# Kernel optimization log

Measured on AMD Instinct MI355X. Metric: run time of the kernel, lower is better.

## Reference

```python
import jax, jax.numpy as jnp
import numpy as np

BETA = 0.1
GAMMA = 0.5
LABEL_SMOOTHING = 0.0
IGNORE_INDEX = -100

B, T, H, V = 8, 512, 2048, 32000  # B = 2 * num_pairs (first half chosen, second half rejected)


def setup_inputs() -> dict:
    key = jax.random.key(0)
    k1, k2, k3, k4 = jax.random.split(key, 4)
    lin_weight = jax.random.normal(k1, (V, H), dtype=jnp.float32) * 0.02
    _input = jax.random.normal(k2, (B, T, H), dtype=jnp.float32)
    target = jax.random.randint(k3, (B, T), 0, V, dtype=jnp.int64)
    # sprinkle some ignore_index positions like padded labels
    pad = jax.random.uniform(k4, (B, T)) < 0.1
    target = jnp.where(pad, IGNORE_INDEX, target)
    bias = jax.random.normal(k4, (V,), dtype=jnp.float32) * 0.02
    return {"lin_weight": lin_weight, "_input": _input, "target": target, "bias": bias}


def reference(lin_weight, _input, target, bias):
    # fused linear -> log_softmax over vocab
    logits = jnp.einsum("bth,vh->btv", _input, lin_weight) + bias  # (B, T, V)
    logps = jax.nn.log_softmax(logits.astype(jnp.float32), axis=-1)
    # gather target log-probs, masking ignore_index
    mask = (target != IGNORE_INDEX)
    tgt = jnp.where(mask, target, 0)
    per_token_logps = jnp.take_along_axis(logps, tgt[..., None], axis=-1)[..., 0]
    per_token_logps = per_token_logps * mask  # (B, T)
    # SimPO uses length-normalized (average) sequence log-prob
    avg_logps = per_token_logps.sum(-1) / jnp.maximum(mask.sum(-1), 1)  # (B,)
    n_pairs = B // 2
    chosen_logps = avg_logps[:n_pairs]
    rejected_logps = avg_logps[n_pairs:]
    d = BETA * (chosen_logps - rejected_logps) - GAMMA
    loss = (-jax.nn.log_sigmoid(d) * (1.0 - LABEL_SMOOTHING)
            - jax.nn.log_sigmoid(-d) * LABEL_SMOOTHING).sum() / n_pairs
    return loss
```

## Files before the change

### kernel.cpp

```cpp
#include <hip/hip_runtime.h>
#include <stdint.h>
#include <math.h>

constexpr int Bb = 8, Tt = 512, Hh = 2048, Vv = 32000;
constexpr int M = Bb * Tt;
constexpr int K = Hh;
constexpr int N = Vv;
constexpr int BM = 256, BN = 256, BK = 64;
constexpr int MBLK = M / BM;
constexpr int NBLK = N / BN;
constexpr int KTILES = K / BK;
constexpr int IGNORE = -100;

typedef __attribute__((ext_vector_type(8))) short bf16x8;
typedef __attribute__((ext_vector_type(4))) float f32x4;
typedef __attribute__((ext_vector_type(4))) unsigned short u16x4;

__device__ inline void gld16(const void* g, void* l) {
  __builtin_amdgcn_global_load_lds(
      (const __attribute__((address_space(1))) uint32_t*)g,
      (__attribute__((address_space(3))) uint32_t*)l, 16, 0, 0);
}

__device__ __forceinline__ void barrier_f() {
  asm volatile("" ::: "memory");
  __builtin_amdgcn_s_barrier();
  asm volatile("" ::: "memory");
}

__device__ inline unsigned short f2bf(float f) {
  union { float f; unsigned u; } x; x.f = f;
  unsigned r = x.u + 0x7fffu + ((x.u >> 16) & 1u);
  return (unsigned short)(r >> 16);
}

constexpr int NX4 = M * K / 4;
constexpr int NW4 = N * K / 4;
__global__ __launch_bounds__(256)
void cast_fused(const float* __restrict__ Xf, unsigned short* __restrict__ Xb,
                const float* __restrict__ Wf, unsigned short* __restrict__ Wb) {
  int64_t i = (int64_t)blockIdx.x * blockDim.x + threadIdx.x;
  const int64_t stride = (int64_t)gridDim.x * blockDim.x;
  for (; i < (int64_t)NX4 + NW4; i += stride) {
    const f32x4* s4;
    u16x4* d4;
    int64_t j;
    if (i < NX4) { s4 = (const f32x4*)Xf; d4 = (u16x4*)Xb; j = i; }
    else         { s4 = (const f32x4*)Wf; d4 = (u16x4*)Wb; j = i - NX4; }
    f32x4 v = __builtin_nontemporal_load(&s4[j]);
    u16x4 o;
    o[0] = f2bf(v[0]); o[1] = f2bf(v[1]); o[2] = f2bf(v[2]); o[3] = f2bf(v[3]);
    d4[j] = o;
  }
}


template <int BUF, int KS, int MH, int VM, class STG>
__device__ __forceinline__ void phase(const unsigned short* __restrict__ AsB,
                                      const unsigned short* __restrict__ BsB,
                                      const int* offA, const int* offB,
                                      bf16x8 (&bfrag)[4], f32x4 (&acc)[8][4],
                                      STG&& stg) {
  const unsigned short* Ab = AsB + (BUF * 2 + KS) * 8192;
  if (MH == 0) {
    const unsigned short* Bp = BsB + (BUF * 2 + KS) * 8192;
#pragma unroll
    for (int nf = 0; nf < 4; ++nf) bfrag[nf] = *(const bf16x8*)(Bp + offB[nf]);
  }
  bf16x8 af[4];
#pragma unroll
  for (int mi = 0; mi < 4; ++mi) af[mi] = *(const bf16x8*)(Ab + offA[MH * 4 + mi]);
  stg();
  if (VM == 8) asm volatile("s_waitcnt vmcnt(8)" ::: "memory");
  if (VM == 4) asm volatile("s_waitcnt vmcnt(4)" ::: "memory");
  if (VM == 0) asm volatile("s_waitcnt vmcnt(0)" ::: "memory");
  barrier_f();
  asm volatile("s_waitcnt lgkmcnt(0)" ::: "memory");
  __builtin_amdgcn_s_setprio(1);
#pragma unroll
  for (int mi = 0; mi < 4; ++mi)
#pragma unroll
    for (int nf = 0; nf < 4; ++nf)
      acc[MH * 4 + mi][nf] = __builtin_amdgcn_mfma_f32_16x16x32_bf16(
          af[mi], bfrag[nf], acc[MH * 4 + mi][nf], 0, 0, 0);
  __builtin_amdgcn_s_setprio(0);
  barrier_f();
}

__global__ __launch_bounds__(512, 2)
void gemm_stats(const unsigned short* __restrict__ X,
                const unsigned short* __restrict__ W,
                const float* __restrict__ bias,
                const int* __restrict__ tgt,
                float* __restrict__ m_part,
                float* __restrict__ s_part,
                float* __restrict__ tlogit) {
  extern __shared__ unsigned short smem[];
  unsigned short* AsB = smem;
  unsigned short* BsB = smem + 32768;
  float* red_m = (float*)(smem + 65536);
  float* red_s = red_m + 1024;

  const int tid = threadIdx.x;
  const int lane = tid & 63;
  const int wid = tid >> 6;
  const int waveM = wid >> 2;
  const int waveN = wid & 3;
  const int q = lane >> 4;
  const int c = lane & 15;

  const int swz = (blockIdx.x & 7) * (MBLK * NBLK / 8) + (blockIdx.x >> 3);
  const int bm = swz & (MBLK - 1);
  const int bn = swz >> 4;

  const int srow = tid >> 2;
  const int sch = (lane & 3) ^ ((lane >> 3) & 3);
  const unsigned short* gA = X + (size_t)(bm * BM + srow) * K + sch * 8;
  const unsigned short* gB = W + (size_t)(bn * BN + srow) * K + sch * 8;
  unsigned short* const dA0 = AsB + wid * 512;
  unsigned short* const dB0 = BsB + wid * 512;

  auto stA = [&](int b, int h, int t) {
    const unsigned short* s = gA + t * BK + h * 32;
    unsigned short* d = dA0 + (b * 2 + h) * 8192;
    gld16(s, d);
    gld16(s + (size_t)128 * K, d + 4096);
  };
  auto stB = [&](int b, int h, int t) {
    const unsigned short* s = gB + t * BK + h * 32;
    unsigned short* d = dB0 + (b * 2 + h) * 8192;
    gld16(s, d);
    gld16(s + (size_t)128 * K, d + 4096);
  };

  const int chrd = (q ^ ((c >> 1) & 3)) * 8;
  int offA[8], offB[4];
#pragma unroll
  for (int mf = 0; mf < 8; ++mf) offA[mf] = (waveM * 128 + mf * 16 + c) * 32 + chrd;
#pragma unroll
  for (int nf = 0; nf < 4; ++nf) offB[nf] = (waveN * 64 + nf * 16 + c) * 32 + chrd;

  f32x4 acc[8][4];
#pragma unroll
  for (int i = 0; i < 8; ++i)
#pragma unroll
    for (int j = 0; j < 4; ++j) acc[i][j] = (f32x4){0.f, 0.f, 0.f, 0.f};
  bf16x8 bfrag[4];

  stA(0, 0, 0); stB(0, 0, 0);
  stA(0, 1, 0); stB(0, 1, 0);
  stA(1, 0, 1); stB(1, 0, 1);
  asm volatile("s_waitcnt vmcnt(8)" ::: "memory");
  barrier_f();

  for (int i = 0; i < KTILES / 2 - 1; ++i) {
    const int t0 = 2 * i;
    phase<0, 0, 0, -1>(AsB, BsB, offA, offB, bfrag, acc, [&] { stA(1, 1, t0 + 1); });
    phase<0, 0, 1,  8>(AsB, BsB, offA, offB, bfrag, acc, [&] { stB(1, 1, t0 + 1); });
    phase<0, 1, 0, -1>(AsB, BsB, offA, offB, bfrag, acc, [&] { stA(0, 0, t0 + 2); });
    phase<0, 1, 1,  8>(AsB, BsB, offA, offB, bfrag, acc, [&] { stB(0, 0, t0 + 2); });
    phase<1, 0, 0, -1>(AsB, BsB, offA, offB, bfrag, acc, [&] { stA(0, 1, t0 + 2); });
    phase<1, 0, 1,  8>(AsB, BsB, offA, offB, bfrag, acc, [&] { stB(0, 1, t0 + 2); });
    phase<1, 1, 0, -1>(AsB, BsB, offA, offB, bfrag, acc, [&] { stA(1, 0, t0 + 3); });
    phase<1, 1, 1,  8>(AsB, BsB, offA, offB, bfrag, acc, [&] { stB(1, 0, t0 + 3); });
  }
  {
    auto nop = [&] {};
    phase<0, 0, 0, -1>(AsB, BsB, offA, offB, bfrag, acc, [&] { stA(1, 1, KTILES - 1); });
    phase<0, 0, 1,  8>(AsB, BsB, offA, offB, bfrag, acc, [&] { stB(1, 1, KTILES - 1); });
    phase<0, 1, 0, -1>(AsB, BsB, offA, offB, bfrag, acc, nop);
    phase<0, 1, 1,  4>(AsB, BsB, offA, offB, bfrag, acc, nop);
    phase<1, 0, 0, -1>(AsB, BsB, offA, offB, bfrag, acc, nop);
    phase<1, 0, 1,  0>(AsB, BsB, offA, offB, bfrag, acc, nop);
    phase<1, 1, 0, -1>(AsB, BsB, offA, offB, bfrag, acc, nop);
    phase<1, 1, 1, -1>(AsB, BsB, offA, offB, bfrag, acc, nop);
  }

  const int colBase = bn * BN + waveN * 64;
  float bvals[4];
#pragma unroll
  for (int nf = 0; nf < 4; ++nf) bvals[nf] = bias[colBase + nf * 16 + c];

#pragma unroll
  for (int mf = 0; mf < 8; ++mf) {
    const int rowBase = bm * BM + waveM * 128 + mf * 16 + q * 4;
#pragma unroll
    for (int reg = 0; reg < 4; ++reg) {
      const int grow = rowBase + reg;
      const int t = tgt[grow];
      float v[4];
      float mloc = -3.4e38f;
#pragma unroll
      for (int nf = 0; nf < 4; ++nf) {
        v[nf] = acc[mf][nf][reg] + bvals[nf];
        mloc = fmaxf(mloc, v[nf]);
        if (colBase + nf * 16 + c == t) tlogit[grow] = v[nf];
      }
#pragma unroll
      for (int off = 1; off < 16; off <<= 1) mloc = fmaxf(mloc, __shfl_xor(mloc, off));
      float sloc = 0.f;
#pragma unroll
      for (int nf = 0; nf < 4; ++nf) sloc += __expf(v[nf] - mloc);
#pragma unroll
      for (int off = 1; off < 16; off <<= 1) sloc += __shfl_xor(sloc, off);
      if (c == 0) {
        const int lrow = waveM * 128 + mf * 16 + q * 4 + reg;
        red_m[waveN * 256 + lrow] = mloc;
        red_s[waveN * 256 + lrow] = sloc;
      }
    }
  }
  __syncthreads();
  if (tid < 256) {
    const float m0 = red_m[tid],       m1 = red_m[256 + tid];
    const float m2 = red_m[512 + tid], m3 = red_m[768 + tid];
    const float mx = fmaxf(fmaxf(m0, m1), fmaxf(m2, m3));
    const float ss = red_s[tid] * __expf(m0 - mx) + red_s[256 + tid] * __expf(m1 - mx) +
                     red_s[512 + tid] * __expf(m2 - mx) + red_s[768 + tid] * __expf(m3 - mx);
    const int grow = bm * BM + tid;
    m_part[(size_t)grow * NBLK + bn] = mx;
    s_part[(size_t)grow * NBLK + bn] = ss;
  }
}

__global__ __launch_bounds__(256)
void combine_rows(const float* __restrict__ m_part, const float* __restrict__ s_part,
                  const float* __restrict__ tlogit, const int* __restrict__ tgt,
                  float* __restrict__ logp) {
  const int row = blockIdx.x * 4 + (threadIdx.x >> 6);
  const int lane = threadIdx.x & 63;
  const float* mrow = m_part + (size_t)row * NBLK;
  const float* srow = s_part + (size_t)row * NBLK;
  const bool v1 = (lane + 64) < NBLK;
  const float m0 = mrow[lane];
  const float s0 = srow[lane];
  const float m1 = v1 ? mrow[lane + 64] : -3.4e38f;
  const float s1 = v1 ? srow[lane + 64] : 0.f;
  float mx = fmaxf(m0, m1);
#pragma unroll
  for (int off = 32; off >= 1; off >>= 1) mx = fmaxf(mx, __shfl_xor(mx, off));
  float s = s0 * __expf(m0 - mx) + s1 * __expf(m1 - mx);
#pragma unroll
  for (int off = 32; off >= 1; off >>= 1) s += __shfl_xor(s, off);
  if (lane == 0) {
    const int t = tgt[row];
    logp[row] = (t == IGNORE) ? 0.f : (tlogit[row] - mx - logf(s));
  }
}

__global__ void finalize(const float* __restrict__ logp, const int* __restrict__ tgt,
                         float* __restrict__ out) {
  __shared__ float avg[8];
  const int w = threadIdx.x >> 6;
  const int lane = threadIdx.x & 63;
  float s = 0.f, cnt = 0.f;
  for (int i = lane; i < Tt; i += 64) {
    const int idx = w * Tt + i;
    s += logp[idx];
    cnt += (tgt[idx] != IGNORE) ? 1.f : 0.f;
  }
#pragma unroll
  for (int off = 32; off >= 1; off >>= 1) {
    s += __shfl_xor(s, off);
    cnt += __shfl_xor(cnt, off);
  }
  if (lane == 0) avg[w] = s / fmaxf(cnt, 1.f);
  __syncthreads();
  if (threadIdx.x == 0) {
    float loss = 0.f;
#pragma unroll
    for (int p = 0; p < 4; ++p) {
      const float d = 0.1f * (avg[p] - avg[p + 4]) - 0.5f;
      const float nl = (d > 0.f) ? log1pf(expf(-d)) : (-d + log1pf(expf(d)));
      loss += nl;
    }
    out[0] = loss * 0.25f;
  }
}

extern "C" void kernel_launch(void* const* d_in, const int* in_sizes, int n_in,
                              void* d_out, int out_size, void* d_ws, size_t ws_size,
                              hipStream_t stream) {
  const float* Wf   = (const float*)d_in[0];
  const float* Xf   = (const float*)d_in[1];
  const int*   tgt  = (const int*)d_in[2];
  const float* bias = (const float*)d_in[3];
  float* out = (float*)d_out;

  char* ws = (char*)d_ws;
  size_t off = 0;
  auto alloc = [&](size_t bytes) {
    void* p = ws + off;
    off += (bytes + 255) & ~(size_t)255;
    return p;
  };
  unsigned short* Xbf = (unsigned short*)alloc((size_t)M * K * 2);
  unsigned short* Wbf = (unsigned short*)alloc((size_t)N * K * 2);
  float* m_part = (float*)alloc((size_t)M * NBLK * 4);
  float* s_part = (float*)alloc((size_t)M * NBLK * 4);
  float* tlog   = (float*)alloc((size_t)M * 4);
  float* logp   = (float*)alloc((size_t)M * 4);

  cast_fused<<<4096, 256, 0, stream>>>(Xf, Xbf, Wf, Wbf);

  constexpr size_t SMEM = 2u * 2u * 256u * 32u * 2u * 2u
                        + 2u * 4u * 256u * 4u;
  gemm_stats<<<dim3(MBLK * NBLK), dim3(512), SMEM, stream>>>(
      Xbf, Wbf, bias, tgt, m_part, s_part, tlog);

  combine_rows<<<M / 4, 256, 0, stream>>>(m_part, s_part, tlog, tgt, logp);
  finalize<<<1, 512, 0, stream>>>(logp, tgt, out);
}
```

Baseline: 917.8 us.

## Software-pipeline LDS fragment reads one phase ahead with inline ds_read_b128

```diff
diff --git a/kernel.cpp b/kernel.cpp
--- a/kernel.cpp
+++ b/kernel.cpp
@@ -26,6 +26,20 @@
   asm volatile("" ::: "memory");
   __builtin_amdgcn_s_barrier();
   asm volatile("" ::: "memory");
+}
+
+template <int IMM>
+__device__ __forceinline__ bf16x8 ds128(uint32_t a) {
+  bf16x8 r;
+  asm volatile("ds_read_b128 %0, %1 offset:%2" : "=v"(r) : "v"(a), "n"(IMM));
+  return r;
+}
+template <int NW>
+__device__ __forceinline__ void wait_lgkm() {
+  if constexpr (NW == 0) asm volatile("s_waitcnt lgkmcnt(0)" ::: "memory");
+  else if constexpr (NW == 4) asm volatile("s_waitcnt lgkmcnt(4)" ::: "memory");
+  else asm volatile("s_waitcnt lgkmcnt(8)" ::: "memory");
+  __builtin_amdgcn_sched_barrier(0);
 }
 
 __device__ inline unsigned short f2bf(float f) {
@@ -55,34 +69,36 @@
 }
 
 
-template <int BUF, int KS, int MH, int VM, class STG>
-__device__ __forceinline__ void phase(const unsigned short* __restrict__ AsB,
-                                      const unsigned short* __restrict__ BsB,
-                                      const int* offA, const int* offB,
-                                      bf16x8 (&bfrag)[4], f32x4 (&acc)[8][4],
+template <int PAR, int MH, int CUR, int NXT, int VM, int LGK, bool LAST, class STG>
+__device__ __forceinline__ void phase(const uint32_t* aA, const uint32_t* aB,
+                                      bf16x8 (&af_lo)[4], bf16x8 (&af_hi)[4],
+                                      bf16x8 (&bfr)[2][4], f32x4 (&acc)[8][4],
                                       STG&& stg) {
-  const unsigned short* Ab = AsB + (BUF * 2 + KS) * 8192;
-  if (MH == 0) {
-    const unsigned short* Bp = BsB + (BUF * 2 + KS) * 8192;
-#pragma unroll
-    for (int nf = 0; nf < 4; ++nf) bfrag[nf] = *(const bf16x8*)(Bp + offB[nf]);
-  }
-  bf16x8 af[4];
-#pragma unroll
-  for (int mi = 0; mi < 4; ++mi) af[mi] = *(const bf16x8*)(Ab + offA[MH * 4 + mi]);
   stg();
-  if (VM == 8) asm volatile("s_waitcnt vmcnt(8)" ::: "memory");
-  if (VM == 4) asm volatile("s_waitcnt vmcnt(4)" ::: "memory");
-  if (VM == 0) asm volatile("s_waitcnt vmcnt(0)" ::: "memory");
+  if constexpr (VM == 8) asm volatile("s_waitcnt vmcnt(8)" ::: "memory");
+  if constexpr (VM == 4) asm volatile("s_waitcnt vmcnt(4)" ::: "memory");
+  if constexpr (VM == 0) asm volatile("s_waitcnt vmcnt(0)" ::: "memory");
   barrier_f();
-  asm volatile("s_waitcnt lgkmcnt(0)" ::: "memory");
+  if constexpr (!LAST) {
+    if constexpr (MH == 0) {
+#pragma unroll
+      for (int i = 0; i < 4; ++i) af_hi[i] = ds128<CUR * 16384>(aA[4 + i]);
+    } else {
+#pragma unroll
+      for (int i = 0; i < 4; ++i) bfr[PAR ^ 1][i] = ds128<NXT * 16384>(aB[i]);
+#pragma unroll
+      for (int i = 0; i < 4; ++i) af_lo[i] = ds128<NXT * 16384>(aA[i]);
+    }
+  }
+  wait_lgkm<LGK>();
   __builtin_amdgcn_s_setprio(1);
 #pragma unroll
   for (int mi = 0; mi < 4; ++mi)
 #pragma unroll
     for (int nf = 0; nf < 4; ++nf)
       acc[MH * 4 + mi][nf] = __builtin_amdgcn_mfma_f32_16x16x32_bf16(
-          af[mi], bfrag[nf], acc[MH * 4 + mi][nf], 0, 0, 0);
+          (MH == 0 ? af_lo : af_hi)[mi], bfr[PAR][nf], acc[MH * 4 + mi][nf],
+          0, 0, 0);
   __builtin_amdgcn_s_setprio(0);
   barrier_f();
 }
@@ -133,47 +149,54 @@
     gld16(s + (size_t)128 * K, d + 4096);
   };
 
+  const uint32_t lds0 = __builtin_amdgcn_groupstaticsize();
   const int chrd = (q ^ ((c >> 1) & 3)) * 8;
-  int offA[8], offB[4];
-#pragma unroll
-  for (int mf = 0; mf < 8; ++mf) offA[mf] = (waveM * 128 + mf * 16 + c) * 32 + chrd;
-#pragma unroll
-  for (int nf = 0; nf < 4; ++nf) offB[nf] = (waveN * 64 + nf * 16 + c) * 32 + chrd;
+  uint32_t aA[8], aB[4];
+#pragma unroll
+  for (int mf = 0; mf < 8; ++mf)
+    aA[mf] = lds0 + 2u * ((waveM * 128 + mf * 16 + c) * 32 + chrd);
+#pragma unroll
+  for (int nf = 0; nf < 4; ++nf)
+    aB[nf] = lds0 + 65536u + 2u * ((waveN * 64 + nf * 16 + c) * 32 + chrd);
 
   f32x4 acc[8][4];
 #pragma unroll
   for (int i = 0; i < 8; ++i)
 #pragma unroll
     for (int j = 0; j < 4; ++j) acc[i][j] = (f32x4){0.f, 0.f, 0.f, 0.f};
-  bf16x8 bfrag[4];
+  bf16x8 af_lo[4], af_hi[4], bfr[2][4];
 
   stA(0, 0, 0); stB(0, 0, 0);
   stA(0, 1, 0); stB(0, 1, 0);
   stA(1, 0, 1); stB(1, 0, 1);
   asm volatile("s_waitcnt vmcnt(8)" ::: "memory");
   barrier_f();
+#pragma unroll
+  for (int i = 0; i < 4; ++i) bfr[0][i] = ds128<0>(aB[i]);
+#pragma unroll
+  for (int i = 0; i < 4; ++i) af_lo[i] = ds128<0>(aA[i]);
 
   for (int i = 0; i < KTILES / 2 - 1; ++i) {
     const int t0 = 2 * i;
-    phase<0, 0, 0, -1>(AsB, BsB, offA, offB, bfrag, acc, [&] { stA(1, 1, t0 + 1); });
-    phase<0, 0, 1,  8>(AsB, BsB, offA, offB, bfrag, acc, [&] { stB(1, 1, t0 + 1); });
-    phase<0, 1, 0, -1>(AsB, BsB, offA, offB, bfrag, acc, [&] { stA(0, 0, t0 + 2); });
-    phase<0, 1, 1,  8>(AsB, BsB, offA, offB, bfrag, acc, [&] { stB(0, 0, t0 + 2); });
-    phase<1, 0, 0, -1>(AsB, BsB, offA, offB, bfrag, acc, [&] { stA(0, 1, t0 + 2); });
-    phase<1, 0, 1,  8>(AsB, BsB, offA, offB, bfrag, acc, [&] { stB(0, 1, t0 + 2); });
-    phase<1, 1, 0, -1>(AsB, BsB, offA, offB, bfrag, acc, [&] { stA(1, 0, t0 + 3); });
-    phase<1, 1, 1,  8>(AsB, BsB, offA, offB, bfrag, acc, [&] { stB(1, 0, t0 + 3); });
+    phase<0, 0, 0, 0, -1, 4, false>(aA, aB, af_lo, af_hi, bfr, acc, [&] { stA(1, 1, t0 + 1); });
+    phase<0, 1, 0, 1,  8, 8, false>(aA, aB, af_lo, af_hi, bfr, acc, [&] { stB(1, 1, t0 + 1); });
+    phase<1, 0, 1, 1, -1, 4, false>(aA, aB, af_lo, af_hi, bfr, acc, [&] { stA(0, 0, t0 + 2); });
+    phase<1, 1, 1, 2,  8, 8, false>(aA, aB, af_lo, af_hi, bfr, acc, [&] { stB(0, 0, t0 + 2); });
+    phase<0, 0, 2, 2, -1, 4, false>(aA, aB, af_lo, af_hi, bfr, acc, [&] { stA(0, 1, t0 + 2); });
+    phase<0, 1, 2, 3,  8, 8, false>(aA, aB, af_lo, af_hi, bfr, acc, [&] { stB(0, 1, t0 + 2); });
+    phase<1, 0, 3, 3, -1, 4, false>(aA, aB, af_lo, af_hi, bfr, acc, [&] { stA(1, 0, t0 + 3); });
+    phase<1, 1, 3, 0,  8, 8, false>(aA, aB, af_lo, af_hi, bfr, acc, [&] { stB(1, 0, t0 + 3); });
   }
   {
     auto nop = [&] {};
-    phase<0, 0, 0, -1>(AsB, BsB, offA, offB, bfrag, acc, [&] { stA(1, 1, KTILES - 1); });
-    phase<0, 0, 1,  8>(AsB, BsB, offA, offB, bfrag, acc, [&] { stB(1, 1, KTILES - 1); });
-    phase<0, 1, 0, -1>(AsB, BsB, offA, offB, bfrag, acc, nop);
-    phase<0, 1, 1,  4>(AsB, BsB, offA, offB, bfrag, acc, nop);
-    phase<1, 0, 0, -1>(AsB, BsB, offA, offB, bfrag, acc, nop);
-    phase<1, 0, 1,  0>(AsB, BsB, offA, offB, bfrag, acc, nop);
-    phase<1, 1, 0, -1>(AsB, BsB, offA, offB, bfrag, acc, nop);
-    phase<1, 1, 1, -1>(AsB, BsB, offA, offB, bfrag, acc, nop);
+    phase<0, 0, 0, 0, -1, 4, false>(aA, aB, af_lo, af_hi, bfr, acc, [&] { stA(1, 1, KTILES - 1); });
+    phase<0, 1, 0, 1,  8, 8, false>(aA, aB, af_lo, af_hi, bfr, acc, [&] { stB(1, 1, KTILES - 1); });
+    phase<1, 0, 1, 1, -1, 4, false>(aA, aB, af_lo, af_hi, bfr, acc, nop);
+    phase<1, 1, 1, 2,  4, 8, false>(aA, aB, af_lo, af_hi, bfr, acc, nop);
+    phase<0, 0, 2, 2, -1, 4, false>(aA, aB, af_lo, af_hi, bfr, acc, nop);
+    phase<0, 1, 2, 3,  0, 8, false>(aA, aB, af_lo, af_hi, bfr, acc, nop);
+    phase<1, 0, 3, 3, -1, 4, false>(aA, aB, af_lo, af_hi, bfr, acc, nop);
+    phase<1, 1, 3, 0, -1, 0, true >(aA, aB, af_lo, af_hi, bfr, acc, nop);
   }
 
   const int colBase = bn * BN + waveN * 64;
```

New measurement: 896.3 us. 1.02x faster.
